# Optimization experiments

Hardware: AMD Instinct MI355X
Metric: run time of the kernel (lower is better)

## Reference

```python
import jax, jax.numpy as jnp
import numpy as np

N, D, K, NUM_CLASSES = 65536, 512, 1024, 2


def setup_inputs() -> dict:
    key = jax.random.key(0)
    kx, kc = jax.random.split(key)
    x = jax.random.normal(kx, (N, D), dtype=jnp.float32)
    codebook_vectors = jax.random.normal(kc, (K, D), dtype=jnp.float32)
    codebook_classes = jnp.arange(K, dtype=jnp.int64 if jax.config.read('jax_enable_x64') else jnp.int32) % NUM_CLASSES
    return {"x": x, "codebook_vectors": codebook_vectors, "codebook_classes": codebook_classes}


def reference(x, codebook_vectors, codebook_classes):
    # Squared Euclidean distances (argmin identical to torch.cdist's p=2 argmin):
    # d2[n,k] = |x_n|^2 - 2 x_n . c_k + |c_k|^2
    x_sq = jnp.sum(x * x, axis=1, keepdims=True)            # (N, 1)
    c_sq = jnp.sum(codebook_vectors * codebook_vectors, axis=1)  # (K,)
    cross = jnp.einsum('nd,kd->nk', x, codebook_vectors)    # (N, K) GEMM
    d2 = x_sq - 2.0 * cross + c_sq[None, :]
    winners = jnp.argmin(d2, axis=1)                         # (N,)
    return codebook_classes[winners]
```

## Files before the change

kernel.cpp:

```cpp
#include <hip/hip_runtime.h>
#include <hip/hip_bf16.h>


#define N_ROWS 65536
#define DIM    512
#define K_CB   1024
#define NT     16
#define LDSBUF_F 16384
#define LDSBUF   32768

typedef short bf16x8 __attribute__((ext_vector_type(8)));
typedef float f32x4  __attribute__((ext_vector_type(4)));
typedef unsigned short u16x8 __attribute__((ext_vector_type(8)));

__device__ __forceinline__ unsigned short f2bf_rn(float f) {
    unsigned u = __float_as_uint(f);
    unsigned r = (u + 0x7FFFu + ((u >> 16) & 1u)) >> 16;
    return (unsigned short)r;
}
__device__ __forceinline__ float bf2f(unsigned short h) {
    return __uint_as_float(((unsigned)h) << 16);
}
__device__ __forceinline__ bf16x8 pack_bf8(float4 a, float4 b) {
    bf16x8 r;
    r[0] = (short)f2bf_rn(a.x); r[1] = (short)f2bf_rn(a.y);
    r[2] = (short)f2bf_rn(a.z); r[3] = (short)f2bf_rn(a.w);
    r[4] = (short)f2bf_rn(b.x); r[5] = (short)f2bf_rn(b.y);
    r[6] = (short)f2bf_rn(b.z); r[7] = (short)f2bf_rn(b.w);
    return r;
}

__device__ __forceinline__ void gload16(const void* g, void* l) {
    __builtin_amdgcn_global_load_lds(
        (const __attribute__((address_space(1))) unsigned int*)g,
        (__attribute__((address_space(3))) unsigned int*)l, 16, 0, 0);
}

__global__ void csq_kernel(const float* __restrict__ C, float* __restrict__ csq) {
    int wid  = (blockIdx.x * blockDim.x + threadIdx.x) >> 6;
    int lane = threadIdx.x & 63;
    const float4* p = (const float4*)(C + (size_t)wid * DIM);
    float4 a = p[lane * 2];
    float4 b = p[lane * 2 + 1];
    float s = a.x*a.x + a.y*a.y + a.z*a.z + a.w*a.w
            + b.x*b.x + b.y*b.y + b.z*b.z + b.w*b.w;
    #pragma unroll
    for (int m = 1; m < 64; m <<= 1) s += __shfl_xor(s, m, 64);
    if (lane == 0) csq[wid] = s;
}

__global__ void split_hi8(const float* __restrict__ src,
                          unsigned short* __restrict__ h, int n8) {
    int stride = gridDim.x * 256;
    for (int i = blockIdx.x * 256 + threadIdx.x; i < n8; i += stride) {
        const float4* p = (const float4*)(src + (size_t)i * 8);
        float4 a = p[0], b = p[1];
        u16x8 o;
        o[0] = f2bf_rn(a.x); o[1] = f2bf_rn(a.y);
        o[2] = f2bf_rn(a.z); o[3] = f2bf_rn(a.w);
        o[4] = f2bf_rn(b.x); o[5] = f2bf_rn(b.y);
        o[6] = f2bf_rn(b.z); o[7] = f2bf_rn(b.w);
        *(u16x8*)(h + (size_t)i * 8) = o;
    }
}

__global__ __launch_bounds__(512, 2)
void gemm_scores(const float* __restrict__ X,
                 const unsigned short* __restrict__ Ch,
                 const float* __restrict__ csq,
                 _Float16* __restrict__ scores) {
    extern __shared__ unsigned short smem[];

    int b  = blockIdx.x;
    int x  = b & 7;
    int m8 = b >> 3;
    int rowtile = x * 32 + (m8 >> 2);
    int coltile = m8 & 3;
    int n0 = rowtile * 256;
    int k0 = coltile * 256;

    int tid  = threadIdx.x;
    int w    = tid >> 6;
    int lane = tid & 63;
    int wr   = w >> 2, wc = w & 3;
    int rbase = wr * 128, cbase = wc * 64;
    int lrow = lane & 15;
    int lk   = lane >> 4;
    int sg   = lk ^ ((lrow >> 1) & 3);

    int arow = tid >> 2;
    int ag   = tid & 3;
    int aswz = (arow >> 1) & 3;
    const float* xsrc0 = X + (size_t)(n0 + arow) * DIM + ag * 8;
    const float* xsrc1 = xsrc0 + (size_t)128 * DIM;
    int adst0 = arow * 32 + (ag ^ aswz) * 8;
    int adst1 = adst0 + 4096;

    int srow = tid >> 2;
    int sgrp = tid & 3;
    int gB   = sgrp ^ ((srow >> 1) & 3);
    size_t oB0 = (size_t)(k0 + srow) * DIM + gB * 8;
    size_t oB1 = oB0 + (size_t)128 * DIM;
    int dB0  = 8192 + w * 512;
    int dB1  = dB0 + 4096;

    f32x4 acc[8][4];
    #pragma unroll
    for (int i = 0; i < 8; i++)
        #pragma unroll
        for (int j = 0; j < 4; j++)
            acc[i][j] = (f32x4){0.f, 0.f, 0.f, 0.f};

    auto issue_B = [&](int tn) {
        unsigned short* bufn = smem + (tn & 1) * LDSBUF_F;
        size_t d = (size_t)tn * 32;
        gload16(Ch + oB0 + d, bufn + dB0);
        gload16(Ch + oB1 + d, bufn + dB1);
    };

    float4 ga0, ga1, gb0, gb1, fa0, fa1, fb0, fb1;

    {
        const float4* p0 = (const float4*)xsrc0;
        const float4* p1 = (const float4*)xsrc1;
        ga0 = p0[0]; ga1 = p0[1]; gb0 = p1[0]; gb1 = p1[1];
        issue_B(0);
        const float4* q0 = (const float4*)(xsrc0 + 32);
        const float4* q1 = (const float4*)(xsrc1 + 32);
        fa0 = q0[0]; fa1 = q0[1]; fb0 = q1[0]; fb1 = q1[1];
        asm volatile("s_waitcnt vmcnt(6)" ::: "memory");
        unsigned short* b0 = smem;
        *(bf16x8*)(b0 + adst0) = pack_bf8(ga0, ga1);
        *(bf16x8*)(b0 + adst1) = pack_bf8(gb0, gb1);
    }

    auto body = [&](int t,
                    float4& ua0, float4& ua1, float4& ub0, float4& ub1,
                    float4& va0, float4& va1, float4& vb0, float4& vb1) {
        if (t + 1 < NT) asm volatile("s_waitcnt vmcnt(4)" ::: "memory");
        else            asm volatile("s_waitcnt vmcnt(0)" ::: "memory");
        asm volatile("s_waitcnt lgkmcnt(0)" ::: "memory");
        __builtin_amdgcn_s_barrier();
        asm volatile("" ::: "memory");

        const unsigned short* buf = smem + (t & 1) * LDSBUF_F;
        const unsigned short* pA = buf + (rbase + lrow) * 32 + sg * 8;
        const unsigned short* pB = buf + 8192 + (cbase + lrow) * 32 + sg * 8;

        bf16x8 bh[4], ah[8];
        #pragma unroll
        for (int n = 0; n < 4; n++) bh[n] = *(const bf16x8*)(pB + n * 512);
        #pragma unroll
        for (int m = 0; m < 8; m++) ah[m] = *(const bf16x8*)(pA + m * 512);

        if (t + 1 < NT) issue_B(t + 1);
        if (t + 2 < NT) {
            const float4* q0 = (const float4*)(xsrc0 + (t + 2) * 32);
            const float4* q1 = (const float4*)(xsrc1 + (t + 2) * 32);
            ua0 = q0[0]; ua1 = q0[1]; ub0 = q1[0]; ub1 = q1[1];
        }

        __builtin_amdgcn_s_setprio(1);
        #pragma unroll
        for (int m = 0; m < 8; m++)
            #pragma unroll
            for (int n = 0; n < 4; n++)
                acc[m][n] = __builtin_amdgcn_mfma_f32_16x16x32_bf16(ah[m], bh[n], acc[m][n], 0, 0, 0);
        __builtin_amdgcn_s_setprio(0);

        if (t + 1 < NT) {
            if (t + 2 < NT) asm volatile("s_waitcnt vmcnt(6)" ::: "memory");
            else            asm volatile("s_waitcnt vmcnt(2)" ::: "memory");
            unsigned short* nb = smem + ((t + 1) & 1) * LDSBUF_F;
            *(bf16x8*)(nb + adst0) = pack_bf8(va0, va1);
            *(bf16x8*)(nb + adst1) = pack_bf8(vb0, vb1);
        }
    };

    for (int tt = 0; tt < NT; tt += 2) {
        body(tt,     ga0, ga1, gb0, gb1, fa0, fa1, fb0, fb1);
        body(tt + 1, fa0, fa1, fb0, fb1, ga0, ga1, gb0, gb1);
    }

    float cs[4];
    #pragma unroll
    for (int n = 0; n < 4; n++) cs[n] = csq[k0 + cbase + n * 16 + lrow];

    #pragma unroll
    for (int m = 0; m < 8; m++) {
        int grow = n0 + rbase + m * 16 + lk * 4;
        #pragma unroll
        for (int r = 0; r < 4; r++) {
            _Float16* sp = scores + (size_t)(grow + r) * K_CB + k0 + cbase + lrow;
            #pragma unroll
            for (int n = 0; n < 4; n++)
                sp[n * 16] = (_Float16)(cs[n] - 2.0f * acc[m][n][r]);
        }
    }
}

struct H8 { _Float16 v[8]; };

__global__ __launch_bounds__(256)
void phase2_kernel(const float* __restrict__ X, const float* __restrict__ C,
                   const float* __restrict__ csq,
                   const _Float16* __restrict__ scores,
                   const int* __restrict__ classes, int* __restrict__ out) {
    int lane = threadIdx.x & 63;
    int n = blockIdx.x * 4 + (threadIdx.x >> 6);

    float s[16];
    {
        const _Float16* sp16 = scores + (size_t)n * K_CB + lane * 16;
        H8 h0 = *(const H8*)sp16;
        H8 h1 = *(const H8*)(sp16 + 8);
        #pragma unroll
        for (int j = 0; j < 8; j++) {
            s[j]     = (float)h0.v[j];
            s[8 + j] = (float)h1.v[j];
        }
    }

    float mn = s[0];
    #pragma unroll
    for (int j = 1; j < 16; j++) mn = fminf(mn, s[j]);
    #pragma unroll
    for (int m = 1; m < 64; m <<= 1) mn = fminf(mn, __shfl_xor(mn, m, 64));

    float thr = mn + 16.0f;
    unsigned fl = 0;
    #pragma unroll
    for (int j = 0; j < 16; j++) fl |= (unsigned)(s[j] <= thr) << j;
    int cnt = __popc(fl);
    #pragma unroll
    for (int m = 1; m < 64; m <<= 1) cnt += __shfl_xor(cnt, m, 64);

    int bestk;
    if (cnt == 1) {
        int kk = 0x7fffffff;
        #pragma unroll
        for (int j = 0; j < 16; j++)
            if ((fl >> j) & 1) kk = lane * 16 + j;
        #pragma unroll
        for (int m = 1; m < 64; m <<= 1) kk = min(kk, __shfl_xor(kk, m, 64));
        bestk = kk;
    } else {
        const float4* xp = (const float4*)(X + (size_t)n * DIM + lane * 8);
        float4 x0 = xp[0], x1 = xp[1];
        float bv = 3.4e38f;
        int bk = 0x7fffffff;
        #pragma unroll 1
        for (int j = 0; j < 16; j++) {
            unsigned long long mask = __ballot((fl >> j) & 1);
            while (mask) {
                int l = __ffsll((unsigned long long)mask) - 1;
                mask &= mask - 1;
                int k = l * 16 + j;
                const float4* cp = (const float4*)(C + (size_t)k * DIM + lane * 8);
                float4 y0 = cp[0], y1 = cp[1];
                float d = x0.x*y0.x + x0.y*y0.y + x0.z*y0.z + x0.w*y0.w
                        + x1.x*y1.x + x1.y*y1.y + x1.z*y1.z + x1.w*y1.w;
                #pragma unroll
                for (int m = 1; m < 64; m <<= 1) d += __shfl_xor(d, m, 64);
                float se = csq[k] - 2.0f * d;
                if (se < bv || (se == bv && k < bk)) { bv = se; bk = k; }
            }
        }
        bestk = bk;
    }
    if (lane == 0) out[n] = classes[bestk];
}

__global__ void init_kernel(unsigned long long* __restrict__ packed) {
    int n = blockIdx.x * 256 + threadIdx.x;
    if (n < N_ROWS) packed[n] = ~0ull;
}

__global__ void split_kernel(const float* __restrict__ src,
                             unsigned short* __restrict__ h,
                             unsigned short* __restrict__ l, int n4) {
    int stride = gridDim.x * 256;
    for (int i = blockIdx.x * 256 + threadIdx.x; i < n4; i += stride) {
        float4 v = ((const float4*)src)[i];
        ushort4 hh, ll;
        float f;
        f = v.x; hh.x = f2bf_rn(f); ll.x = f2bf_rn(f - bf2f(hh.x));
        f = v.y; hh.y = f2bf_rn(f); ll.y = f2bf_rn(f - bf2f(hh.y));
        f = v.z; hh.z = f2bf_rn(f); ll.z = f2bf_rn(f - bf2f(hh.z));
        f = v.w; hh.w = f2bf_rn(f); ll.w = f2bf_rn(f - bf2f(hh.w));
        ((ushort4*)h)[i] = hh;
        ((ushort4*)l)[i] = ll;
    }
}

__global__ __launch_bounds__(512, 2)
void gemm_argmin(const unsigned short* __restrict__ Xh,
                 const unsigned short* __restrict__ Xl,
                 const unsigned short* __restrict__ Ch,
                 const unsigned short* __restrict__ Cl,
                 const float* __restrict__ csq,
                 unsigned long long* __restrict__ packed) {
    extern __shared__ unsigned short smem[];

    int b  = blockIdx.x;
    int x  = b & 7;
    int m8 = b >> 3;
    int rowtile = x * 32 + (m8 >> 2);
    int coltile = m8 & 3;
    int n0 = rowtile * 256;
    int k0 = coltile * 256;

    int tid  = threadIdx.x;
    int w    = tid >> 6;
    int lane = tid & 63;
    int wr   = w >> 2, wc = w & 3;
    int rbase = wr * 128, cbase = wc * 64;
    int lrow = lane & 15;
    int lk   = lane >> 4;
    int sg   = lk ^ ((lrow >> 1) & 3);

    int srow = tid >> 2;
    int sgrp = tid & 3;
    int r1   = (srow < 64) ? srow : srow + 64;
    int ggA  = sgrp ^ ((r1 >> 1) & 3);
    int gB   = sgrp ^ ((srow >> 1) & 3);
    size_t oA1 = (size_t)(n0 + r1) * DIM + ggA * 8;
    size_t oA2 = oA1 + (size_t)64 * DIM;
    size_t oB0 = (size_t)(k0 + srow) * DIM + gB * 8;
    size_t oB1 = oB0 + (size_t)128 * DIM;
    int rowA1_0 = (w < 4) ? w * 16 : w * 16 + 64;
    int dA1  = rowA1_0 * 32;
    int dA2  = dA1 + 2048;
    int dB0  = 16384 + w * 512;
    int dB1  = dB0 + 4096;
    int dBl0 = dB0 + 8192;
    int dBl1 = dB1 + 8192;

    f32x4 acc[8][4];
    #pragma unroll
    for (int i = 0; i < 8; i++)
        #pragma unroll
        for (int j = 0; j < 4; j++)
            acc[i][j] = (f32x4){0.f, 0.f, 0.f, 0.f};

    bf16x8 bh[4], bl[4];

    auto issue_tile = [&](int t) {
        unsigned short* bufn = smem + (t & 1) * LDSBUF;
        size_t d = (size_t)t * 32;
        gload16(Xh + oA1 + d, bufn + dA1);
        gload16(Xl + oA1 + d, bufn + 8192 + dA1);
        gload16(Ch + oB0 + d, bufn + dB0);
        gload16(Ch + oB1 + d, bufn + dB1);
        gload16(Cl + oB0 + d, bufn + dBl0);
        gload16(Cl + oB1 + d, bufn + dBl1);
        gload16(Xh + oA2 + d, bufn + dA2);
        gload16(Xl + oA2 + d, bufn + 8192 + dA2);
    };

    auto mfma_half = [&](int mb, const bf16x8* ah, const bf16x8* al) {
        __builtin_amdgcn_s_setprio(1);
        #pragma unroll
        for (int mm = 0; mm < 4; mm++)
            #pragma unroll
            for (int n = 0; n < 4; n++)
                acc[mb + mm][n] = __builtin_amdgcn_mfma_f32_16x16x32_bf16(ah[mm], bh[n], acc[mb + mm][n], 0, 0, 0);
        #pragma unroll
        for (int mm = 0; mm < 4; mm++)
            #pragma unroll
            for (int n = 0; n < 4; n++)
                acc[mb + mm][n] = __builtin_amdgcn_mfma_f32_16x16x32_bf16(ah[mm], bl[n], acc[mb + mm][n], 0, 0, 0);
        #pragma unroll
        for (int mm = 0; mm < 4; mm++)
            #pragma unroll
            for (int n = 0; n < 4; n++)
                acc[mb + mm][n] = __builtin_amdgcn_mfma_f32_16x16x32_bf16(al[mm], bh[n], acc[mb + mm][n], 0, 0, 0);
        __builtin_amdgcn_s_setprio(0);
    };

    issue_tile(0);

    for (int t = 0; t < NT; ++t) {
        asm volatile("s_waitcnt vmcnt(0)" ::: "memory");
        __builtin_amdgcn_s_barrier();
        asm volatile("" ::: "memory");

        const unsigned short* buf = smem + (t & 1) * LDSBUF;
        const unsigned short* pA = buf + (rbase + lrow) * 32 + sg * 8;
        const unsigned short* pB = buf + 16384 + (cbase + lrow) * 32 + sg * 8;

        #pragma unroll
        for (int n = 0; n < 4; n++) {
            bh[n] = *(const bf16x8*)(pB + n * 512);
            bl[n] = *(const bf16x8*)(pB + 8192 + n * 512);
        }
        bf16x8 ah[4], al[4];
        #pragma unroll
        for (int mm = 0; mm < 4; mm++) {
            ah[mm] = *(const bf16x8*)(pA + mm * 512);
            al[mm] = *(const bf16x8*)(pA + 8192 + mm * 512);
        }
        if (t + 1 < NT) issue_tile(t + 1);

        mfma_half(0, ah, al);

        bf16x8 ah2[4], al2[4];
        #pragma unroll
        for (int mm = 0; mm < 4; mm++) {
            ah2[mm] = *(const bf16x8*)(pA + (4 + mm) * 512);
            al2[mm] = *(const bf16x8*)(pA + 8192 + (4 + mm) * 512);
        }
        mfma_half(4, ah2, al2);
    }

    float cs[4];
    #pragma unroll
    for (int n = 0; n < 4; n++) cs[n] = csq[k0 + cbase + n * 16 + lrow];

    #pragma unroll
    for (int m = 0; m < 8; m++) {
        #pragma unroll
        for (int r = 0; r < 4; r++) {
            unsigned long long best = ~0ull;
            #pragma unroll
            for (int n = 0; n < 4; n++) {
                float s = cs[n] - 2.0f * acc[m][n][r];
                unsigned kb  = __float_as_uint(s);
                unsigned key = kb ^ (unsigned)(((int)kb >> 31) | 0x80000000);
                unsigned col = (unsigned)(k0 + cbase + n * 16 + lrow);
                unsigned long long pk = (((unsigned long long)key) << 32) | col;
                best = pk < best ? pk : best;
            }
            #pragma unroll
            for (int mask = 1; mask <= 8; mask <<= 1) {
                unsigned hi = __shfl_xor((unsigned)(best >> 32), mask, 64);
                unsigned lo = __shfl_xor((unsigned)(best & 0xFFFFFFFFu), mask, 64);
                unsigned long long other = (((unsigned long long)hi) << 32) | lo;
                best = other < best ? other : best;
            }
            if (lrow == 0) {
                int grow = n0 + rbase + m * 16 + lk * 4 + r;
                atomicMin(&packed[grow], best);
            }
        }
    }
}

__global__ void map_kernel(const unsigned long long* __restrict__ packed,
                           const int* __restrict__ classes,
                           int* __restrict__ out) {
    int n = blockIdx.x * 256 + threadIdx.x;
    if (n < N_ROWS) {
        unsigned col = (unsigned)(packed[n] & 0xFFFFFFFFull);
        out[n] = classes[col];
    }
}

extern "C" void kernel_launch(void* const* d_in, const int* in_sizes, int n_in,
                              void* d_out, int out_size, void* d_ws, size_t ws_size,
                              hipStream_t stream) {
    const float* X       = (const float*)d_in[0];
    const float* C       = (const float*)d_in[1];
    const int*   classes = (const int*)d_in[2];
    int*         out     = (int*)d_out;
    char* ws = (char*)d_ws;

    {
        size_t off = 0;
        float* csq = (float*)(ws + off);                  off += 4096;
        unsigned short* Ch = (unsigned short*)(ws + off); off += (size_t)K_CB * DIM * 2;
        _Float16* scores = (_Float16*)(ws + off);         off += (size_t)N_ROWS * K_CB * 2;
        if (ws_size >= off) {
            csq_kernel<<<K_CB / 4, 256, 0, stream>>>(C, csq);
            split_hi8<<<256, 256, 0, stream>>>(C, Ch, K_CB * DIM / 8);
            hipFuncSetAttribute((const void*)gemm_scores,
                                hipFuncAttributeMaxDynamicSharedMemorySize,
                                2 * LDSBUF_F * (int)sizeof(unsigned short));
            gemm_scores<<<(N_ROWS / 256) * (K_CB / 256), 512,
                          2 * LDSBUF_F * sizeof(unsigned short), stream>>>(
                X, Ch, csq, scores);
            phase2_kernel<<<N_ROWS / 4, 256, 0, stream>>>(X, C, csq, scores, classes, out);
            return;
        }
    }

    size_t off = 0;
    unsigned long long* packed = (unsigned long long*)(ws + off); off += (size_t)N_ROWS * 8;
    float* csq = (float*)(ws + off);                              off += (size_t)K_CB * 4;
    unsigned short* Xh = (unsigned short*)(ws + off);             off += (size_t)N_ROWS * DIM * 2;
    unsigned short* Xl = (unsigned short*)(ws + off);             off += (size_t)N_ROWS * DIM * 2;
    unsigned short* Ch = (unsigned short*)(ws + off);             off += (size_t)K_CB * DIM * 2;
    unsigned short* Cl = (unsigned short*)(ws + off);             off += (size_t)K_CB * DIM * 2;

    init_kernel<<<N_ROWS / 256, 256, 0, stream>>>(packed);
    csq_kernel<<<K_CB / 4, 256, 0, stream>>>(C, csq);
    split_kernel<<<2048, 256, 0, stream>>>(X, Xh, Xl, N_ROWS * DIM / 4);
    split_kernel<<<512, 256, 0, stream>>>(C, Ch, Cl, K_CB * DIM / 4);
    hipFuncSetAttribute((const void*)gemm_argmin,
                        hipFuncAttributeMaxDynamicSharedMemorySize,
                        2 * LDSBUF * (int)sizeof(unsigned short));
    gemm_argmin<<<(N_ROWS / 256) * (K_CB / 256), 512,
                  2 * LDSBUF * sizeof(unsigned short), stream>>>(
        Xh, Xl, Ch, Cl, csq, packed);
    map_kernel<<<N_ROWS / 256, 256, 0, stream>>>(packed, classes, out);
}
```

Before: 158.1 us.

## Replace full fp16 score matrix with per-row candidate lists via atomics

The GEMM epilogue no longer writes the full N×K fp16 score matrix. It computes a per-tile row minimum through LDS and appends only scores within a threshold of it to a small per-row candidate buffer, using an atomic counter per row. Phase 2 reads these candidates, refines ambiguous rows with exact fp32 dot products, and falls back to a full scan when a row overflows its slots. This removes roughly 128MB of score write and read traffic, at the cost of atomics, an extra LDS reduction pass and a counter-init kernel. Because the threshold is relative to each column tile's local minimum, some tiles will write extra candidates.

```diff
diff --git a/kernel.cpp b/kernel.cpp
--- a/kernel.cpp
+++ b/kernel.cpp
@@ -8,6 +8,8 @@
 #define NT     16
 #define LDSBUF_F 16384
 #define LDSBUF   32768
+#define SLOTS  16
+#define THR    16.0f
 
 typedef short bf16x8 __attribute__((ext_vector_type(8)));
 typedef float f32x4  __attribute__((ext_vector_type(4)));
@@ -29,11 +31,23 @@
     r[6] = (short)f2bf_rn(b.z); r[7] = (short)f2bf_rn(b.w);
     return r;
 }
+__device__ __forceinline__ unsigned fkey(float s) {
+    unsigned kb = __float_as_uint(s);
+    return kb ^ (unsigned)(((int)kb >> 31) | 0x80000000);
+}
+__device__ __forceinline__ float unfkey(unsigned key) {
+    unsigned m2 = ((int)key < 0) ? 0x80000000u : 0xFFFFFFFFu;
+    return __uint_as_float(key ^ m2);
+}
 
 __device__ __forceinline__ void gload16(const void* g, void* l) {
     __builtin_amdgcn_global_load_lds(
         (const __attribute__((address_space(1))) unsigned int*)g,
         (__attribute__((address_space(3))) unsigned int*)l, 16, 0, 0);
+}
+
+__global__ void init_cnt(int* __restrict__ cnt) {
+    cnt[blockIdx.x * 256 + threadIdx.x] = 0;
 }
 
 __global__ void csq_kernel(const float* __restrict__ C, float* __restrict__ csq) {
@@ -65,10 +79,10 @@
 }
 
 __global__ __launch_bounds__(512, 2)
-void gemm_scores(const float* __restrict__ X,
-                 const unsigned short* __restrict__ Ch,
-                 const float* __restrict__ csq,
-                 _Float16* __restrict__ scores) {
+void gemm_cand(const float* __restrict__ X,
+               const unsigned short* __restrict__ Ch,
+               const float* __restrict__ csq,
+               int* __restrict__ cnt, uint2* __restrict__ cand) {
     extern __shared__ unsigned short smem[];
 
     int b  = blockIdx.x;
@@ -186,76 +200,90 @@
     #pragma unroll
     for (int n = 0; n < 4; n++) cs[n] = csq[k0 + cbase + n * 16 + lrow];
 
+    __syncthreads();
+    float* lmin = (float*)smem;
+
     #pragma unroll
     for (int m = 0; m < 8; m++) {
-        int grow = n0 + rbase + m * 16 + lk * 4;
         #pragma unroll
         for (int r = 0; r < 4; r++) {
-            _Float16* sp = scores + (size_t)(grow + r) * K_CB + k0 + cbase + lrow;
+            float mn = 3.4e38f;
             #pragma unroll
             for (int n = 0; n < 4; n++)
-                sp[n * 16] = (_Float16)(cs[n] - 2.0f * acc[m][n][r]);
-        }
-    }
-}
-
-struct H8 { _Float16 v[8]; };
+                mn = fminf(mn, cs[n] - 2.0f * acc[m][n][r]);
+            #pragma unroll
+            for (int mask = 1; mask <= 8; mask <<= 1)
+                mn = fminf(mn, __shfl_xor(mn, mask, 64));
+            if (lrow == 0) {
+                int row_l = rbase + m * 16 + lk * 4 + r;
+                lmin[row_l * 4 + wc] = mn;
+            }
+        }
+    }
+    __syncthreads();
+
+    #pragma unroll
+    for (int m = 0; m < 8; m++) {
+        #pragma unroll
+        for (int r = 0; r < 4; r++) {
+            int row_l = rbase + m * 16 + lk * 4 + r;
+            f32x4 v = *(const f32x4*)&lmin[row_l * 4];
+            float bm = fminf(fminf(v[0], v[1]), fminf(v[2], v[3]));
+            float thr = bm + THR;
+            int grow = n0 + row_l;
+            #pragma unroll
+            for (int n = 0; n < 4; n++) {
+                float s = cs[n] - 2.0f * acc[m][n][r];
+                if (s <= thr) {
+                    int idx = atomicAdd(&cnt[grow], 1);
+                    if (idx < SLOTS) {
+                        uint2 e;
+                        e.x = fkey(s);
+                        e.y = (unsigned)(k0 + cbase + n * 16 + lrow);
+                        cand[(size_t)grow * SLOTS + idx] = e;
+                    }
+                }
+            }
+        }
+    }
+}
 
 __global__ __launch_bounds__(256)
 void phase2_kernel(const float* __restrict__ X, const float* __restrict__ C,
                    const float* __restrict__ csq,
-                   const _Float16* __restrict__ scores,
+                   const int* __restrict__ cnt, const uint2* __restrict__ cand,
                    const int* __restrict__ classes, int* __restrict__ out) {
     int lane = threadIdx.x & 63;
     int n = blockIdx.x * 4 + (threadIdx.x >> 6);
 
-    float s[16];
-    {
-        const _Float16* sp16 = scores + (size_t)n * K_CB + lane * 16;
-        H8 h0 = *(const H8*)sp16;
-        H8 h1 = *(const H8*)(sp16 + 8);
-        #pragma unroll
-        for (int j = 0; j < 8; j++) {
-            s[j]     = (float)h0.v[j];
-            s[8 + j] = (float)h1.v[j];
-        }
-    }
-
-    float mn = s[0];
-    #pragma unroll
-    for (int j = 1; j < 16; j++) mn = fminf(mn, s[j]);
-    #pragma unroll
-    for (int m = 1; m < 64; m <<= 1) mn = fminf(mn, __shfl_xor(mn, m, 64));
-
-    float thr = mn + 16.0f;
-    unsigned fl = 0;
-    #pragma unroll
-    for (int j = 0; j < 16; j++) fl |= (unsigned)(s[j] <= thr) << j;
-    int cnt = __popc(fl);
-    #pragma unroll
-    for (int m = 1; m < 64; m <<= 1) cnt += __shfl_xor(cnt, m, 64);
-
+    int c = cnt[n];
     int bestk;
-    if (cnt == 1) {
-        int kk = 0x7fffffff;
-        #pragma unroll
-        for (int j = 0; j < 16; j++)
-            if ((fl >> j) & 1) kk = lane * 16 + j;
-        #pragma unroll
-        for (int m = 1; m < 64; m <<= 1) kk = min(kk, __shfl_xor(kk, m, 64));
-        bestk = kk;
-    } else {
-        const float4* xp = (const float4*)(X + (size_t)n * DIM + lane * 8);
-        float4 x0 = xp[0], x1 = xp[1];
-        float bv = 3.4e38f;
-        int bk = 0x7fffffff;
-        #pragma unroll 1
-        for (int j = 0; j < 16; j++) {
-            unsigned long long mask = __ballot((fl >> j) & 1);
-            while (mask) {
-                int l = __ffsll((unsigned long long)mask) - 1;
-                mask &= mask - 1;
-                int k = l * 16 + j;
+    if (c <= SLOTS) {
+        uint2 e;
+        if (lane < c) e = cand[(size_t)n * SLOTS + lane];
+        else { e.x = 0xFFFFFFFFu; e.y = 0x7FFFFFFFu; }
+
+        unsigned mk = e.x;
+        #pragma unroll
+        for (int m = 1; m < 64; m <<= 1) mk = min(mk, __shfl_xor(mk, m, 64));
+        float smin = unfkey(mk);
+        float thr = smin + THR;
+        float sv = unfkey(e.x);
+        bool flag = (lane < c) && (sv <= thr);
+        unsigned long long bal = __ballot(flag);
+
+        if (__popcll(bal) == 1) {
+            int src = __ffsll(bal) - 1;
+            bestk = __shfl((int)e.y, src, 64);
+        } else {
+            const float4* xp = (const float4*)(X + (size_t)n * DIM + lane * 8);
+            float4 x0 = xp[0], x1 = xp[1];
+            float bv = 3.4e38f;
+            int bk = 0x7fffffff;
+            while (bal) {
+                int l = __ffsll(bal) - 1;
+                bal &= bal - 1;
+                int k = __shfl((int)e.y, l, 64);
                 const float4* cp = (const float4*)(C + (size_t)k * DIM + lane * 8);
                 float4 y0 = cp[0], y1 = cp[1];
                 float d = x0.x*y0.x + x0.y*y0.y + x0.z*y0.z + x0.w*y0.w
@@ -265,6 +293,22 @@
                 float se = csq[k] - 2.0f * d;
                 if (se < bv || (se == bv && k < bk)) { bv = se; bk = k; }
             }
+            bestk = bk;
+        }
+    } else {
+        const float4* xp = (const float4*)(X + (size_t)n * DIM + lane * 8);
+        float4 x0 = xp[0], x1 = xp[1];
+        float bv = 3.4e38f;
+        int bk = 0x7fffffff;
+        for (int k = 0; k < K_CB; ++k) {
+            const float4* cp = (const float4*)(C + (size_t)k * DIM + lane * 8);
+            float4 y0 = cp[0], y1 = cp[1];
+            float d = x0.x*y0.x + x0.y*y0.y + x0.z*y0.z + x0.w*y0.w
+                    + x1.x*y1.x + x1.y*y1.y + x1.z*y1.z + x1.w*y1.w;
+            #pragma unroll
+            for (int m = 1; m < 64; m <<= 1) d += __shfl_xor(d, m, 64);
+            float se = csq[k] - 2.0f * d;
+            if (se < bv) { bv = se; bk = k; }
         }
         bestk = bk;
     }
@@ -469,17 +513,19 @@
         size_t off = 0;
         float* csq = (float*)(ws + off);                  off += 4096;
         unsigned short* Ch = (unsigned short*)(ws + off); off += (size_t)K_CB * DIM * 2;
-        _Float16* scores = (_Float16*)(ws + off);         off += (size_t)N_ROWS * K_CB * 2;
+        int* cnt = (int*)(ws + off);                      off += (size_t)N_ROWS * 4;
+        uint2* cand = (uint2*)(ws + off);                 off += (size_t)N_ROWS * SLOTS * 8;
         if (ws_size >= off) {
+            init_cnt<<<N_ROWS / 256, 256, 0, stream>>>(cnt);
             csq_kernel<<<K_CB / 4, 256, 0, stream>>>(C, csq);
             split_hi8<<<256, 256, 0, stream>>>(C, Ch, K_CB * DIM / 8);
-            hipFuncSetAttribute((const void*)gemm_scores,
+            hipFuncSetAttribute((const void*)gemm_cand,
                                 hipFuncAttributeMaxDynamicSharedMemorySize,
                                 2 * LDSBUF_F * (int)sizeof(unsigned short));
-            gemm_scores<<<(N_ROWS / 256) * (K_CB / 256), 512,
-                          2 * LDSBUF_F * sizeof(unsigned short), stream>>>(
-                X, Ch, csq, scores);
-            phase2_kernel<<<N_ROWS / 4, 256, 0, stream>>>(X, C, csq, scores, classes, out);
+            gemm_cand<<<(N_ROWS / 256) * (K_CB / 256), 512,
+                        2 * LDSBUF_F * sizeof(unsigned short), stream>>>(
+                X, Ch, csq, cnt, cand);
+            phase2_kernel<<<N_ROWS / 4, 256, 0, stream>>>(X, C, csq, cnt, cand, classes, out);
             return;
         }
     }
```

Result: slower. 525.5 us (+232.3%).
